# Optimization experiments

Hardware: AMD Instinct MI355X
Metric: run time of the kernel (lower is better)

## Reference

```python
import jax, jax.numpy as jnp
import numpy as np

V = 100000   # num_vertices
E = 3200000  # directed edges (symmetric: both directions of E//2 undirected edges)
B = 8        # batch of meshes
C = 3        # xyz vertex features


def setup_inputs() -> dict:
    key = jax.random.key(0)
    k1, k2, k3, k4 = jax.random.split(key, 4)
    src = jax.random.randint(k1, (E // 2,), 0, V, dtype=jnp.int32)
    dst = jax.random.randint(k2, (E // 2,), 0, V, dtype=jnp.int32)
    edge_index = jnp.stack([jnp.concatenate([src, dst]),
                            jnp.concatenate([dst, src])])  # (2, E)
    features = jax.random.normal(k3, (B, V, C), dtype=jnp.float32)
    target_features = jax.random.normal(k4, (B, V, C), dtype=jnp.float32)
    return {"features": features, "target_features": target_features,
            "edge_index": edge_index}


def _sym_laplacian(edge_index, num_nodes, dtype):
    """get_laplacian(..., normalization='sym'): L = I - D^{-1/2} A D^{-1/2}.
    Returns (lap_row, lap_col, lap_weight) as edge list with self-loops appended."""
    row, col = edge_index
    ones = jnp.ones(row.shape, dtype)
    deg = jax.ops.segment_sum(ones, row, num_segments=num_nodes)
    deg_inv_sqrt = jnp.where(deg > 0, deg, 1.0) ** -0.5
    deg_inv_sqrt = jnp.where(deg > 0, deg_inv_sqrt, 0.0)
    ew = -deg_inv_sqrt[row] * deg_inv_sqrt[col]
    loop = jnp.arange(num_nodes, dtype=row.dtype)
    lap_row = jnp.concatenate([row, loop])
    lap_col = jnp.concatenate([col, loop])
    lap_w = jnp.concatenate([ew, jnp.ones((num_nodes,), dtype)])
    return lap_row, lap_col, lap_w


def _apply_laplacian(x, lap_row, lap_col, lap_w, num_nodes):
    # x: (B, V, C) -> gather on source vertex, scale, scatter_add on target vertex
    xt = jnp.swapaxes(x, 0, 1)                       # (V, B, C)
    msg = xt[lap_row] * lap_w[:, None, None]          # (E+V, B, C)
    out = jax.ops.segment_sum(msg, lap_col, num_segments=num_nodes)  # (V, B, C)
    return jnp.swapaxes(out, 0, 1)                    # (B, V, C)


def reference(features, target_features, edge_index):
    lap_row, lap_col, lap_w = _sym_laplacian(edge_index, V, features.dtype)
    lap_x = _apply_laplacian(features, lap_row, lap_col, lap_w, V)
    lap_y = _apply_laplacian(target_features, lap_row, lap_col, lap_w, V)
    # per-batch mse averaged over batch == global mean since shapes are uniform
    return jnp.mean((lap_x - lap_y) ** 2)
```

## Files before the change

kernel.cpp:

```cpp
#include <hip/hip_runtime.h>

#define C_CONST 3
#define B_CONST 8
#define BC 24
#define NCH 3
#define VP 196
#define NP 512
#define CAP 6784
#define K1_T 1024
#define K1_EPT 16
#define K1_EPB (K1_T * K1_EPT)
#define GT 576
#define KREG 12

typedef float floatx2 __attribute__((ext_vector_type(2)));

__global__ __launch_bounds__(1024) void bucket_kernel(
    const int* __restrict__ row, const int* __restrict__ col, int E,
    int* __restrict__ pcount, unsigned int* __restrict__ bucket)
{
    __shared__ unsigned int sl[K1_EPB];
    __shared__ int hist[NP];
    __shared__ int offs[NP];
    __shared__ int gbase[NP];
    __shared__ int scanbuf[NP];
    int tid = threadIdx.x;
    for (int i = tid; i < NP; i += K1_T) hist[i] = 0;
    __syncthreads();

    int e0 = blockIdx.x * K1_EPB + tid * K1_EPT;
    unsigned int pk[K1_EPT];
    int pe[K1_EPT];
    int rk[K1_EPT];
    if (e0 + K1_EPT <= E) {
        int rs[K1_EPT], cs[K1_EPT];
#pragma unroll
        for (int q = 0; q < K1_EPT / 4; q++) {
            int4 rv = *(const int4*)(row + e0 + q * 4);
            int4 cv = *(const int4*)(col + e0 + q * 4);
            rs[q*4+0] = rv.x; rs[q*4+1] = rv.y; rs[q*4+2] = rv.z; rs[q*4+3] = rv.w;
            cs[q*4+0] = cv.x; cs[q*4+1] = cv.y; cs[q*4+2] = cv.z; cs[q*4+3] = cv.w;
        }
#pragma unroll
        for (int i = 0; i < K1_EPT; i++) {
            int c = cs[i];
            int p = c / VP;
            pe[i] = p;
            pk[i] = (unsigned int)rs[i] | ((unsigned int)(c - p * VP) << 17);
        }
    } else {
#pragma unroll
        for (int i = 0; i < K1_EPT; i++) {
            int e = e0 + i;
            if (e < E) {
                int c = col[e];
                int p = c / VP;
                pe[i] = p;
                pk[i] = (unsigned int)row[e] | ((unsigned int)(c - p * VP) << 17);
            } else { pe[i] = -1; pk[i] = 0; }
        }
    }
#pragma unroll
    for (int i = 0; i < K1_EPT; i++)
        rk[i] = (pe[i] >= 0) ? atomicAdd(&hist[pe[i]], 1) : 0;
    __syncthreads();

    if (tid < NP) scanbuf[tid] = hist[tid];
    __syncthreads();
    for (int off = 1; off < NP; off <<= 1) {
        int t2 = (tid < NP && tid >= off) ? scanbuf[tid - off] : 0;
        __syncthreads();
        if (tid < NP) scanbuf[tid] += t2;
        __syncthreads();
    }
    if (tid < NP) {
        offs[tid] = scanbuf[tid] - hist[tid];
        gbase[tid] = (hist[tid] > 0) ? atomicAdd(&pcount[tid], hist[tid]) : 0;
    }
    __syncthreads();

#pragma unroll
    for (int i = 0; i < K1_EPT; i++)
        if (pe[i] >= 0) sl[offs[pe[i]] + rk[i]] = pk[i];
    __syncthreads();

    int wid = tid >> 6;
    int lane = tid & 63;
    for (int pp = wid * (NP / 16); pp < (wid + 1) * (NP / 16); pp++) {
        int cnt = hist[pp];
        int lo = offs[pp];
        int gb = gbase[pp];
        unsigned int* dst = bucket + (size_t)pp * CAP;
        for (int i = lane; i < cnt; i += 64) {
            int pos = gb + i;
            if (pos < CAP) dst[pos] = sl[lo + i];
        }
    }
}

#define PREP_T 1024
__global__ __launch_bounds__(1024) void prep_kernel(
    const int* __restrict__ pcount, const unsigned int* __restrict__ bucket,
    const float* __restrict__ x, const float* __restrict__ y, int V,
    unsigned char* __restrict__ wh)
{
    __shared__ int cnt[VP];
    __shared__ float ssc[VP];
    __shared__ unsigned char tile[VP * BC];
    int p = blockIdx.x;
    int tid = threadIdx.x;
    for (int i = tid; i < VP; i += PREP_T) cnt[i] = 0;
    __syncthreads();
    int n = pcount[p]; if (n > CAP) n = CAP;
    const unsigned int* bp = bucket + (size_t)p * CAP;
    for (int i = tid; i < n; i += PREP_T) atomicAdd(&cnt[bp[i] >> 17], 1);
    __syncthreads();
    int vb = p * VP;
    int nv = V - vb; if (nv > VP) nv = VP; if (nv < 0) nv = 0;
    for (int i = tid; i < nv; i += PREP_T) {
        int dg = cnt[i];
        ssc[i] = (dg > 0) ? rsqrtf((float)dg) : 1.0f;
    }
    __syncthreads();

    int ns = nv * C_CONST;
    int ns4 = ns >> 2;
    for (int idx = tid; idx < B_CONST * ns4; idx += PREP_T) {
        int b = idx / ns4;
        int q = idx - b * ns4;
        size_t off = ((size_t)b * V + vb) * C_CONST + (size_t)q * 4;
        float4 xv = *(const float4*)(x + off);
        float4 yv = *(const float4*)(y + off);
        float vals[4] = {xv.x - yv.x, xv.y - yv.y, xv.z - yv.z, xv.w - yv.w};
        int f0 = q * 4;
#pragma unroll
        for (int j = 0; j < 4; j++) {
            int f = f0 + j;
            int vl = f / C_CONST;
            int c = f - vl * C_CONST;
            float w = ssc[vl] * vals[j];
            int packed = __builtin_amdgcn_cvt_pk_fp8_f32(w, w, 0, false);
            tile[vl * BC + b * C_CONST + c] = (unsigned char)(packed & 0xFF);
        }
    }
    __syncthreads();

    int nbytes = nv * BC;
    uint4* dst = (uint4*)(wh + (size_t)vb * BC);
    const uint4* srcT = (const uint4*)tile;
    for (int i = tid; i < (nbytes >> 4); i += PREP_T) dst[i] = srcT[i];
}

__global__ __launch_bounds__(GT) void gather_loss_kernel(
    const int* __restrict__ pcount, const unsigned int* __restrict__ bucket,
    const uint2* __restrict__ whp, int V, float inv_n, float* __restrict__ out)
{
    __shared__ unsigned int sorted[CAP];
    __shared__ int rowptr[VP + 1];
    __shared__ int cur[VP];
    __shared__ int scanbuf[256];
    __shared__ float ls[16];
    int p = blockIdx.x;
    int tid = threadIdx.x;
    int n = pcount[p]; if (n > CAP) n = CAP;
    const unsigned int* bp = bucket + (size_t)p * CAP;

    unsigned int ent[KREG];
#pragma unroll
    for (int k = 0; k < KREG; k++) {
        int i = tid + k * GT;
        ent[k] = (i < n) ? bp[i] : 0xFFFFFFFFu;
    }

    for (int i = tid; i < VP; i += GT) cur[i] = 0;
    __syncthreads();
#pragma unroll
    for (int k = 0; k < KREG; k++)
        if (ent[k] != 0xFFFFFFFFu) atomicAdd(&cur[ent[k] >> 17], 1);
    __syncthreads();

    if (tid < 256) scanbuf[tid] = (tid < VP) ? cur[tid] : 0;
    __syncthreads();
    for (int off = 1; off < 256; off <<= 1) {
        int t2 = (tid < 256 && tid >= off) ? scanbuf[tid - off] : 0;
        __syncthreads();
        if (tid < 256) scanbuf[tid] += t2;
        __syncthreads();
    }
    if (tid == 0) rowptr[0] = 0;
    if (tid < VP) rowptr[tid + 1] = scanbuf[tid];
    for (int i = tid; i < VP; i += GT) cur[i] = 0;
    __syncthreads();

#pragma unroll
    for (int k = 0; k < KREG; k++) {
        unsigned int e = ent[k];
        if (e != 0xFFFFFFFFu) {
            int cl = e >> 17;
            int slot = rowptr[cl] + atomicAdd(&cur[cl], 1);
            sorted[slot] = e & 0x1FFFFu;
        }
    }
    __syncthreads();

    float s = 0.0f;
    for (int item = tid; item < VP * NCH; item += GT) {
        int cl = item / NCH;
        int j = item - cl * NCH;
        int v = p * VP + cl;
        if (v < V) {
            int q0 = rowptr[cl], q1 = rowptr[cl + 1];
            int dg = q1 - q0;
            float a0=0.f,a1=0.f,a2=0.f,a3=0.f,a4=0.f,a5=0.f,a6=0.f,a7=0.f;
            for (int q = q0; q < q1; q++) {
                int r = (int)sorted[q];
                uint2 u = whp[r * NCH + j];
                floatx2 f0 = __builtin_amdgcn_cvt_pk_f32_fp8((int)u.x, false);
                floatx2 f1 = __builtin_amdgcn_cvt_pk_f32_fp8((int)u.x, true);
                floatx2 f2 = __builtin_amdgcn_cvt_pk_f32_fp8((int)u.y, false);
                floatx2 f3 = __builtin_amdgcn_cvt_pk_f32_fp8((int)u.y, true);
                a0 += f0.x; a1 += f0.y; a2 += f1.x; a3 += f1.y;
                a4 += f2.x; a5 += f2.y; a6 += f3.x; a7 += f3.y;
            }
            float dvv = (dg > 0) ? rsqrtf((float)dg) : 0.0f;
            float di  = (dg > 0) ? sqrtf((float)dg)  : 1.0f;
            uint2 su = whp[v * NCH + j];
            floatx2 s0 = __builtin_amdgcn_cvt_pk_f32_fp8((int)su.x, false);
            floatx2 s1 = __builtin_amdgcn_cvt_pk_f32_fp8((int)su.x, true);
            floatx2 s2 = __builtin_amdgcn_cvt_pk_f32_fp8((int)su.y, false);
            floatx2 s3 = __builtin_amdgcn_cvt_pk_f32_fp8((int)su.y, true);
            float r0 = s0.x * di - dvv * a0;
            float r1 = s0.y * di - dvv * a1;
            float r2 = s1.x * di - dvv * a2;
            float r3 = s1.y * di - dvv * a3;
            float r4 = s2.x * di - dvv * a4;
            float r5 = s2.y * di - dvv * a5;
            float r6 = s3.x * di - dvv * a6;
            float r7 = s3.y * di - dvv * a7;
            s += r0*r0 + r1*r1 + r2*r2 + r3*r3 + r4*r4 + r5*r5 + r6*r6 + r7*r7;
        }
    }

    for (int off = 32; off > 0; off >>= 1) s += __shfl_down(s, off, 64);
    int lane = tid & 63;
    int wid  = tid >> 6;
    if (lane == 0) ls[wid] = s;
    __syncthreads();
    if (tid == 0) {
        float tot = 0.0f;
        for (int i = 0; i < (GT >> 6); i++) tot += ls[i];
        atomicAdd(out, tot * inv_n);
    }
}

extern "C" void kernel_launch(void* const* d_in, const int* in_sizes, int n_in,
                              void* d_out, int out_size, void* d_ws, size_t ws_size,
                              hipStream_t stream) {
    const float* x = (const float*)d_in[0];
    const float* y = (const float*)d_in[1];
    const int*  ei = (const int*)d_in[2];

    const int E = in_sizes[2] / 2;
    const int V = in_sizes[0] / (B_CONST * C_CONST);
    const int* row = ei;
    const int* col = ei + E;

    char* ws = (char*)d_ws;
    size_t off = 0;
    unsigned int* bucket = (unsigned int*)(ws + off); off += (size_t)NP * CAP * 4;
    unsigned char* wh = (unsigned char*)(ws + off);   off += (size_t)NP * VP * BC;
    int*   pcount = (int*)(ws + off);    off += (size_t)NP * 4;
    float* outf = (float*)d_out;

    hipMemsetAsync(pcount, 0, (size_t)NP * sizeof(int), stream);
    hipMemsetAsync(d_out, 0, sizeof(float), stream);

    bucket_kernel<<<(E + K1_EPB - 1) / K1_EPB, K1_T, 0, stream>>>(row, col, E, pcount, bucket);
    prep_kernel<<<NP, PREP_T, 0, stream>>>(pcount, bucket, x, y, V, wh);
    gather_loss_kernel<<<NP, GT, 0, stream>>>(pcount, bucket, (const uint2*)wh, V,
                                              1.0f / (float)(V * BC), outf);
}
```

Measured before the change: 142.3 us.

## Fuse bucket, prep and gather-loss stages into one cooperative kernel with grid syncs

Replaces the three separate kernel launches with a single cooperative kernel of 256 blocks of 1024 threads. The stages are separated by grid-wide syncs, and each block handles two vertex partitions in the prep and gather stages. The goal is to remove launch gaps and inter-kernel drain. In exchange it adds grid barrier cost, lowers the block count, and loses the coalesced int4 edge loads in the bucketing stage.

After: 217.1 us. 1.53x slower.

```diff
diff --git a/kernel.cpp b/kernel.cpp
--- a/kernel.cpp
+++ b/kernel.cpp
@@ -1,255 +1,248 @@
 #include <hip/hip_runtime.h>
+#include <hip/hip_cooperative_groups.h>
+
+namespace cg = cooperative_groups;
 
 #define C_CONST 3
 #define B_CONST 8
 #define BC 24
 #define NCH 3
 #define VP 196
+#define VP2 392
 #define NP 512
 #define CAP 6784
-#define K1_T 1024
-#define K1_EPT 16
-#define K1_EPB (K1_T * K1_EPT)
-#define GT 576
-#define KREG 12
+#define GRID 256
+#define TPB 1024
+#define EPB 12500
+#define EPT 13
+#define KREG 14
+
+#define SMEM_BYTES 59536
 
 typedef float floatx2 __attribute__((ext_vector_type(2)));
 
-__global__ __launch_bounds__(1024) void bucket_kernel(
+__global__ __launch_bounds__(TPB) void fused_kernel(
     const int* __restrict__ row, const int* __restrict__ col, int E,
-    int* __restrict__ pcount, unsigned int* __restrict__ bucket)
+    int* __restrict__ pcount, unsigned int* __restrict__ bucket,
+    const float* __restrict__ x, const float* __restrict__ y, int V,
+    unsigned char* __restrict__ wh, float* __restrict__ out, float inv_n)
 {
-    __shared__ unsigned int sl[K1_EPB];
-    __shared__ int hist[NP];
-    __shared__ int offs[NP];
-    __shared__ int gbase[NP];
-    __shared__ int scanbuf[NP];
-    int tid = threadIdx.x;
-    for (int i = tid; i < NP; i += K1_T) hist[i] = 0;
-    __syncthreads();
-
-    int e0 = blockIdx.x * K1_EPB + tid * K1_EPT;
-    unsigned int pk[K1_EPT];
-    int pe[K1_EPT];
-    int rk[K1_EPT];
-    if (e0 + K1_EPT <= E) {
-        int rs[K1_EPT], cs[K1_EPT];
-#pragma unroll
-        for (int q = 0; q < K1_EPT / 4; q++) {
-            int4 rv = *(const int4*)(row + e0 + q * 4);
-            int4 cv = *(const int4*)(col + e0 + q * 4);
-            rs[q*4+0] = rv.x; rs[q*4+1] = rv.y; rs[q*4+2] = rv.z; rs[q*4+3] = rv.w;
-            cs[q*4+0] = cv.x; cs[q*4+1] = cv.y; cs[q*4+2] = cv.z; cs[q*4+3] = cv.w;
-        }
-#pragma unroll
-        for (int i = 0; i < K1_EPT; i++) {
-            int c = cs[i];
-            int p = c / VP;
-            pe[i] = p;
-            pk[i] = (unsigned int)rs[i] | ((unsigned int)(c - p * VP) << 17);
-        }
-    } else {
-#pragma unroll
-        for (int i = 0; i < K1_EPT; i++) {
-            int e = e0 + i;
-            if (e < E) {
+    __shared__ __align__(16) unsigned char smem[SMEM_BYTES];
+    cg::grid_group gg = cg::this_grid();
+    const int tid = threadIdx.x;
+    const int b = blockIdx.x;
+
+    {
+        unsigned int* sl = (unsigned int*)smem;
+        int* hist  = (int*)(smem + 50000);
+        int* offs  = (int*)(smem + 52048);
+        int* gbase = (int*)(smem + 54096);
+        int* scan  = (int*)(smem + 56144);
+        for (int i = tid; i < NP; i += TPB) hist[i] = 0;
+        __syncthreads();
+
+        const int ebase = b * EPB;
+        unsigned int pk[EPT]; int pe[EPT]; int rk[EPT];
+#pragma unroll
+        for (int k = 0; k < EPT; k++) {
+            int idx = tid + k * TPB;
+            int e = ebase + idx;
+            if (idx < EPB && e < E) {
                 int c = col[e];
                 int p = c / VP;
-                pe[i] = p;
-                pk[i] = (unsigned int)row[e] | ((unsigned int)(c - p * VP) << 17);
-            } else { pe[i] = -1; pk[i] = 0; }
+                pe[k] = p;
+                pk[k] = (unsigned int)row[e] | ((unsigned int)(c - p * VP) << 17);
+            } else { pe[k] = -1; pk[k] = 0; }
+        }
+#pragma unroll
+        for (int k = 0; k < EPT; k++)
+            rk[k] = (pe[k] >= 0) ? atomicAdd(&hist[pe[k]], 1) : 0;
+        __syncthreads();
+
+        if (tid < NP) scan[tid] = hist[tid];
+        __syncthreads();
+        for (int off = 1; off < NP; off <<= 1) {
+            int t2 = (tid < NP && tid >= off) ? scan[tid - off] : 0;
+            __syncthreads();
+            if (tid < NP) scan[tid] += t2;
+            __syncthreads();
+        }
+        if (tid < NP) {
+            offs[tid] = scan[tid] - hist[tid];
+            gbase[tid] = (hist[tid] > 0) ? atomicAdd(&pcount[tid], hist[tid]) : 0;
+        }
+        __syncthreads();
+#pragma unroll
+        for (int k = 0; k < EPT; k++)
+            if (pe[k] >= 0) sl[offs[pe[k]] + rk[k]] = pk[k];
+        __syncthreads();
+
+        int wid = tid >> 6, lane = tid & 63;
+        for (int pp = wid * (NP / 16); pp < (wid + 1) * (NP / 16); pp++) {
+            int cnt = hist[pp], lo = offs[pp], gb = gbase[pp];
+            unsigned int* dst = bucket + (size_t)pp * CAP;
+            for (int i = lane; i < cnt; i += 64) {
+                int pos = gb + i;
+                if (pos < CAP) dst[pos] = sl[lo + i];
+            }
         }
     }
-#pragma unroll
-    for (int i = 0; i < K1_EPT; i++)
-        rk[i] = (pe[i] >= 0) ? atomicAdd(&hist[pe[i]], 1) : 0;
-    __syncthreads();
-
-    if (tid < NP) scanbuf[tid] = hist[tid];
-    __syncthreads();
-    for (int off = 1; off < NP; off <<= 1) {
-        int t2 = (tid < NP && tid >= off) ? scanbuf[tid - off] : 0;
-        __syncthreads();
-        if (tid < NP) scanbuf[tid] += t2;
-        __syncthreads();
+
+    gg.sync();
+
+    const int p0 = b, p1 = b + GRID;
+    const int vb0 = p0 * VP, vb1 = p1 * VP;
+    int nv0 = V - vb0; nv0 = nv0 < 0 ? 0 : (nv0 > VP ? VP : nv0);
+    int nv1 = V - vb1; nv1 = nv1 < 0 ? 0 : (nv1 > VP ? VP : nv1);
+    int n0 = pcount[p0]; n0 = n0 > CAP ? CAP : n0;
+    int n1 = pcount[p1]; n1 = n1 > CAP ? CAP : n1;
+    const unsigned int* bp0 = bucket + (size_t)p0 * CAP;
+    const unsigned int* bp1 = bucket + (size_t)p1 * CAP;
+    {
+        int* cnt = (int*)smem;
+        float* ssc = (float*)(smem + 1568);
+        unsigned char* tile = smem + 3136;
+        for (int i = tid; i < VP2; i += TPB) cnt[i] = 0;
+        __syncthreads();
+        for (int i = tid; i < n0; i += TPB) atomicAdd(&cnt[bp0[i] >> 17], 1);
+        for (int i = tid; i < n1; i += TPB) atomicAdd(&cnt[VP + (bp1[i] >> 17)], 1);
+        __syncthreads();
+        for (int i = tid; i < VP2; i += TPB) {
+            int dg = cnt[i];
+            ssc[i] = (dg > 0) ? rsqrtf((float)dg) : 1.0f;
+        }
+        __syncthreads();
+#pragma unroll
+        for (int h = 0; h < 2; h++) {
+            int vb = h ? vb1 : vb0;
+            int nv = h ? nv1 : nv0;
+            int ns4 = (nv * C_CONST) >> 2;
+            for (int idx = tid; idx < B_CONST * ns4; idx += TPB) {
+                int b8 = idx / ns4;
+                int q = idx - b8 * ns4;
+                size_t off = ((size_t)b8 * V + vb) * C_CONST + (size_t)q * 4;
+                float4 xv = *(const float4*)(x + off);
+                float4 yv = *(const float4*)(y + off);
+                float vals[4] = {xv.x - yv.x, xv.y - yv.y, xv.z - yv.z, xv.w - yv.w};
+                int f0 = q * 4;
+#pragma unroll
+                for (int j = 0; j < 4; j++) {
+                    int f = f0 + j;
+                    int vl = f / C_CONST;
+                    int c = f - vl * C_CONST;
+                    float w = ssc[h * VP + vl] * vals[j];
+                    int packed = __builtin_amdgcn_cvt_pk_fp8_f32(w, w, 0, false);
+                    tile[(h * VP + vl) * BC + b8 * C_CONST + c] = (unsigned char)(packed & 0xFF);
+                }
+            }
+        }
+        __syncthreads();
+#pragma unroll
+        for (int h = 0; h < 2; h++) {
+            int vb = h ? vb1 : vb0;
+            int nv = h ? nv1 : nv0;
+            int nbytes = nv * BC;
+            uint4* dst = (uint4*)(wh + (size_t)vb * BC);
+            const uint4* srcT = (const uint4*)(tile + h * VP * BC);
+            for (int i = tid; i < (nbytes >> 4); i += TPB) dst[i] = srcT[i];
+        }
     }
-    if (tid < NP) {
-        offs[tid] = scanbuf[tid] - hist[tid];
-        gbase[tid] = (hist[tid] > 0) ? atomicAdd(&pcount[tid], hist[tid]) : 0;
-    }
-    __syncthreads();
-
-#pragma unroll
-    for (int i = 0; i < K1_EPT; i++)
-        if (pe[i] >= 0) sl[offs[pe[i]] + rk[i]] = pk[i];
-    __syncthreads();
-
-    int wid = tid >> 6;
-    int lane = tid & 63;
-    for (int pp = wid * (NP / 16); pp < (wid + 1) * (NP / 16); pp++) {
-        int cnt = hist[pp];
-        int lo = offs[pp];
-        int gb = gbase[pp];
-        unsigned int* dst = bucket + (size_t)pp * CAP;
-        for (int i = lane; i < cnt; i += 64) {
-            int pos = gb + i;
-            if (pos < CAP) dst[pos] = sl[lo + i];
-        }
-    }
-}
-
-#define PREP_T 1024
-__global__ __launch_bounds__(1024) void prep_kernel(
-    const int* __restrict__ pcount, const unsigned int* __restrict__ bucket,
-    const float* __restrict__ x, const float* __restrict__ y, int V,
-    unsigned char* __restrict__ wh)
-{
-    __shared__ int cnt[VP];
-    __shared__ float ssc[VP];
-    __shared__ unsigned char tile[VP * BC];
-    int p = blockIdx.x;
-    int tid = threadIdx.x;
-    for (int i = tid; i < VP; i += PREP_T) cnt[i] = 0;
-    __syncthreads();
-    int n = pcount[p]; if (n > CAP) n = CAP;
-    const unsigned int* bp = bucket + (size_t)p * CAP;
-    for (int i = tid; i < n; i += PREP_T) atomicAdd(&cnt[bp[i] >> 17], 1);
-    __syncthreads();
-    int vb = p * VP;
-    int nv = V - vb; if (nv > VP) nv = VP; if (nv < 0) nv = 0;
-    for (int i = tid; i < nv; i += PREP_T) {
-        int dg = cnt[i];
-        ssc[i] = (dg > 0) ? rsqrtf((float)dg) : 1.0f;
-    }
-    __syncthreads();
-
-    int ns = nv * C_CONST;
-    int ns4 = ns >> 2;
-    for (int idx = tid; idx < B_CONST * ns4; idx += PREP_T) {
-        int b = idx / ns4;
-        int q = idx - b * ns4;
-        size_t off = ((size_t)b * V + vb) * C_CONST + (size_t)q * 4;
-        float4 xv = *(const float4*)(x + off);
-        float4 yv = *(const float4*)(y + off);
-        float vals[4] = {xv.x - yv.x, xv.y - yv.y, xv.z - yv.z, xv.w - yv.w};
-        int f0 = q * 4;
-#pragma unroll
-        for (int j = 0; j < 4; j++) {
-            int f = f0 + j;
-            int vl = f / C_CONST;
-            int c = f - vl * C_CONST;
-            float w = ssc[vl] * vals[j];
-            int packed = __builtin_amdgcn_cvt_pk_fp8_f32(w, w, 0, false);
-            tile[vl * BC + b * C_CONST + c] = (unsigned char)(packed & 0xFF);
-        }
-    }
-    __syncthreads();
-
-    int nbytes = nv * BC;
-    uint4* dst = (uint4*)(wh + (size_t)vb * BC);
-    const uint4* srcT = (const uint4*)tile;
-    for (int i = tid; i < (nbytes >> 4); i += PREP_T) dst[i] = srcT[i];
-}
-
-__global__ __launch_bounds__(GT) void gather_loss_kernel(
-    const int* __restrict__ pcount, const unsigned int* __restrict__ bucket,
-    const uint2* __restrict__ whp, int V, float inv_n, float* __restrict__ out)
-{
-    __shared__ unsigned int sorted[CAP];
-    __shared__ int rowptr[VP + 1];
-    __shared__ int cur[VP];
-    __shared__ int scanbuf[256];
-    __shared__ float ls[16];
-    int p = blockIdx.x;
-    int tid = threadIdx.x;
-    int n = pcount[p]; if (n > CAP) n = CAP;
-    const unsigned int* bp = bucket + (size_t)p * CAP;
-
-    unsigned int ent[KREG];
-#pragma unroll
-    for (int k = 0; k < KREG; k++) {
-        int i = tid + k * GT;
-        ent[k] = (i < n) ? bp[i] : 0xFFFFFFFFu;
-    }
-
-    for (int i = tid; i < VP; i += GT) cur[i] = 0;
-    __syncthreads();
-#pragma unroll
-    for (int k = 0; k < KREG; k++)
-        if (ent[k] != 0xFFFFFFFFu) atomicAdd(&cur[ent[k] >> 17], 1);
-    __syncthreads();
-
-    if (tid < 256) scanbuf[tid] = (tid < VP) ? cur[tid] : 0;
-    __syncthreads();
-    for (int off = 1; off < 256; off <<= 1) {
-        int t2 = (tid < 256 && tid >= off) ? scanbuf[tid - off] : 0;
-        __syncthreads();
-        if (tid < 256) scanbuf[tid] += t2;
-        __syncthreads();
-    }
-    if (tid == 0) rowptr[0] = 0;
-    if (tid < VP) rowptr[tid + 1] = scanbuf[tid];
-    for (int i = tid; i < VP; i += GT) cur[i] = 0;
-    __syncthreads();
-
-#pragma unroll
-    for (int k = 0; k < KREG; k++) {
-        unsigned int e = ent[k];
-        if (e != 0xFFFFFFFFu) {
-            int cl = e >> 17;
-            int slot = rowptr[cl] + atomicAdd(&cur[cl], 1);
-            sorted[slot] = e & 0x1FFFFu;
-        }
-    }
-    __syncthreads();
-
-    float s = 0.0f;
-    for (int item = tid; item < VP * NCH; item += GT) {
-        int cl = item / NCH;
-        int j = item - cl * NCH;
-        int v = p * VP + cl;
-        if (v < V) {
-            int q0 = rowptr[cl], q1 = rowptr[cl + 1];
-            int dg = q1 - q0;
-            float a0=0.f,a1=0.f,a2=0.f,a3=0.f,a4=0.f,a5=0.f,a6=0.f,a7=0.f;
-            for (int q = q0; q < q1; q++) {
-                int r = (int)sorted[q];
-                uint2 u = whp[r * NCH + j];
-                floatx2 f0 = __builtin_amdgcn_cvt_pk_f32_fp8((int)u.x, false);
-                floatx2 f1 = __builtin_amdgcn_cvt_pk_f32_fp8((int)u.x, true);
-                floatx2 f2 = __builtin_amdgcn_cvt_pk_f32_fp8((int)u.y, false);
-                floatx2 f3 = __builtin_amdgcn_cvt_pk_f32_fp8((int)u.y, true);
-                a0 += f0.x; a1 += f0.y; a2 += f1.x; a3 += f1.y;
-                a4 += f2.x; a5 += f2.y; a6 += f3.x; a7 += f3.y;
-            }
-            float dvv = (dg > 0) ? rsqrtf((float)dg) : 0.0f;
-            float di  = (dg > 0) ? sqrtf((float)dg)  : 1.0f;
-            uint2 su = whp[v * NCH + j];
-            floatx2 s0 = __builtin_amdgcn_cvt_pk_f32_fp8((int)su.x, false);
-            floatx2 s1 = __builtin_amdgcn_cvt_pk_f32_fp8((int)su.x, true);
-            floatx2 s2 = __builtin_amdgcn_cvt_pk_f32_fp8((int)su.y, false);
-            floatx2 s3 = __builtin_amdgcn_cvt_pk_f32_fp8((int)su.y, true);
-            float r0 = s0.x * di - dvv * a0;
-            float r1 = s0.y * di - dvv * a1;
-            float r2 = s1.x * di - dvv * a2;
-            float r3 = s1.y * di - dvv * a3;
-            float r4 = s2.x * di - dvv * a4;
-            float r5 = s2.y * di - dvv * a5;
-            float r6 = s3.x * di - dvv * a6;
-            float r7 = s3.y * di - dvv * a7;
-            s += r0*r0 + r1*r1 + r2*r2 + r3*r3 + r4*r4 + r5*r5 + r6*r6 + r7*r7;
-        }
-    }
-
-    for (int off = 32; off > 0; off >>= 1) s += __shfl_down(s, off, 64);
-    int lane = tid & 63;
-    int wid  = tid >> 6;
-    if (lane == 0) ls[wid] = s;
-    __syncthreads();
-    if (tid == 0) {
-        float tot = 0.0f;
-        for (int i = 0; i < (GT >> 6); i++) tot += ls[i];
-        atomicAdd(out, tot * inv_n);
+
+    gg.sync();
+
+    {
+        unsigned int* sorted = (unsigned int*)smem;
+        int* rowptr = (int*)(smem + 54272);
+        int* cur    = (int*)(smem + 55844);
+        int* scan   = (int*)(smem + 57412);
+        float* ls   = (float*)(smem + 59460);
+        const int n = n0 + n1;
+
+        unsigned int ent[KREG];
+#pragma unroll
+        for (int k = 0; k < KREG; k++) {
+            int i = tid + k * TPB;
+            unsigned int e = 0xFFFFFFFFu;
+            if (i < n0) e = bp0[i];
+            else if (i < n) e = bp1[i - n0] + ((unsigned int)VP << 17);
+            ent[k] = e;
+        }
+        for (int i = tid; i < VP2; i += TPB) cur[i] = 0;
+        __syncthreads();
+#pragma unroll
+        for (int k = 0; k < KREG; k++)
+            if (ent[k] != 0xFFFFFFFFu) atomicAdd(&cur[ent[k] >> 17], 1);
+        __syncthreads();
+        if (tid < NP) scan[tid] = (tid < VP2) ? cur[tid] : 0;
+        __syncthreads();
+        for (int off = 1; off < NP; off <<= 1) {
+            int t2 = (tid < NP && tid >= off) ? scan[tid - off] : 0;
+            __syncthreads();
+            if (tid < NP) scan[tid] += t2;
+            __syncthreads();
+        }
+        if (tid == 0) rowptr[0] = 0;
+        if (tid < VP2) rowptr[tid + 1] = scan[tid];
+        for (int i = tid; i < VP2; i += TPB) cur[i] = 0;
+        __syncthreads();
+#pragma unroll
+        for (int k = 0; k < KREG; k++) {
+            unsigned int e = ent[k];
+            if (e != 0xFFFFFFFFu) {
+                int cl = e >> 17;
+                int slot = rowptr[cl] + atomicAdd(&cur[cl], 1);
+                sorted[slot] = e & 0x1FFFFu;
+            }
+        }
+        __syncthreads();
+
+        const uint2* whp = (const uint2*)wh;
+        float s = 0.0f;
+        for (int item = tid; item < VP2 * NCH; item += TPB) {
+            int cl = item / NCH;
+            int j = item - cl * NCH;
+            int v = (cl < VP) ? (vb0 + cl) : (vb1 + cl - VP);
+            if (v < V) {
+                int q0 = rowptr[cl], q1 = rowptr[cl + 1];
+                int dg = q1 - q0;
+                float a0=0.f,a1=0.f,a2=0.f,a3=0.f,a4=0.f,a5=0.f,a6=0.f,a7=0.f;
+                for (int q = q0; q < q1; q++) {
+                    int r = (int)sorted[q];
+                    uint2 u = whp[r * NCH + j];
+                    floatx2 f0 = __builtin_amdgcn_cvt_pk_f32_fp8((int)u.x, false);
+                    floatx2 f1 = __builtin_amdgcn_cvt_pk_f32_fp8((int)u.x, true);
+                    floatx2 f2 = __builtin_amdgcn_cvt_pk_f32_fp8((int)u.y, false);
+                    floatx2 f3 = __builtin_amdgcn_cvt_pk_f32_fp8((int)u.y, true);
+                    a0 += f0.x; a1 += f0.y; a2 += f1.x; a3 += f1.y;
+                    a4 += f2.x; a5 += f2.y; a6 += f3.x; a7 += f3.y;
+                }
+                float dvv = (dg > 0) ? rsqrtf((float)dg) : 0.0f;
+                float di  = (dg > 0) ? sqrtf((float)dg)  : 1.0f;
+                uint2 su = whp[v * NCH + j];
+                floatx2 s0 = __builtin_amdgcn_cvt_pk_f32_fp8((int)su.x, false);
+                floatx2 s1 = __builtin_amdgcn_cvt_pk_f32_fp8((int)su.x, true);
+                floatx2 s2 = __builtin_amdgcn_cvt_pk_f32_fp8((int)su.y, false);
+                floatx2 s3 = __builtin_amdgcn_cvt_pk_f32_fp8((int)su.y, true);
+                float r0 = s0.x * di - dvv * a0;
+                float r1 = s0.y * di - dvv * a1;
+                float r2 = s1.x * di - dvv * a2;
+                float r3 = s1.y * di - dvv * a3;
+                float r4 = s2.x * di - dvv * a4;
+                float r5 = s2.y * di - dvv * a5;
+                float r6 = s3.x * di - dvv * a6;
+                float r7 = s3.y * di - dvv * a7;
+                s += r0*r0 + r1*r1 + r2*r2 + r3*r3 + r4*r4 + r5*r5 + r6*r6 + r7*r7;
+            }
+        }
+        for (int off = 32; off > 0; off >>= 1) s += __shfl_down(s, off, 64);
+        int lane = tid & 63, wid = tid >> 6;
+        if (lane == 0) ls[wid] = s;
+        __syncthreads();
+        if (tid == 0) {
+            float tot = 0.0f;
+            for (int i = 0; i < TPB / 64; i++) tot += ls[i];
+            atomicAdd(out, tot * inv_n);
+        }
     }
 }
 
@@ -269,14 +262,15 @@
     size_t off = 0;
     unsigned int* bucket = (unsigned int*)(ws + off); off += (size_t)NP * CAP * 4;
     unsigned char* wh = (unsigned char*)(ws + off);   off += (size_t)NP * VP * BC;
-    int*   pcount = (int*)(ws + off);    off += (size_t)NP * 4;
+    int* pcount = (int*)(ws + off);                   off += (size_t)NP * 4;
     float* outf = (float*)d_out;
 
     hipMemsetAsync(pcount, 0, (size_t)NP * sizeof(int), stream);
     hipMemsetAsync(d_out, 0, sizeof(float), stream);
 
-    bucket_kernel<<<(E + K1_EPB - 1) / K1_EPB, K1_T, 0, stream>>>(row, col, E, pcount, bucket);
-    prep_kernel<<<NP, PREP_T, 0, stream>>>(pcount, bucket, x, y, V, wh);
-    gather_loss_kernel<<<NP, GT, 0, stream>>>(pcount, bucket, (const uint2*)wh, V,
-                                              1.0f / (float)(V * BC), outf);
+    int Ei = E, Vi = V;
+    float inv_n = 1.0f / (float)(V * BC);
+    void* args[] = {(void*)&row, (void*)&col, (void*)&Ei, (void*)&pcount, (void*)&bucket,
+                    (void*)&x, (void*)&y, (void*)&Vi, (void*)&wh, (void*)&outf, (void*)&inv_n};
+    hipLaunchCooperativeKernel((void*)fused_kernel, dim3(GRID), dim3(TPB), args, 0, stream);
 }
```

## Split per-vertex gather across two lanes and retune bucket/gather block sizes

Applied to the files above, without the earlier changes.

The gather-loss kernel now gives each (vertex, channel) item to two adjacent lanes, which each sum half the neighbour list and combine partial sums with a shuffle. The inner loop is unrolled by two so more loads are in flight, and the block size goes from 576 to 1024 threads with fewer register-held entries per thread. The bucket kernel drops to 512 threads so each thread owns one partition, and it does the histogram atomics inline while packing partition and rank into one word to save registers. The aim is more memory parallelism and less divergence from uneven degrees, at the cost of extra shuffles and half-idle lanes in the final step.

Result: faster. 138.9 us (-2.4%).

```diff
diff --git a/kernel.cpp b/kernel.cpp
--- a/kernel.cpp
+++ b/kernel.cpp
@@ -7,15 +7,15 @@
 #define VP 196
 #define NP 512
 #define CAP 6784
-#define K1_T 1024
+#define K1_T 512
 #define K1_EPT 16
 #define K1_EPB (K1_T * K1_EPT)
-#define GT 576
-#define KREG 12
+#define GT 1024
+#define KREG 7
 
 typedef float floatx2 __attribute__((ext_vector_type(2)));
 
-__global__ __launch_bounds__(1024) void bucket_kernel(
+__global__ __launch_bounds__(K1_T) void bucket_kernel(
     const int* __restrict__ row, const int* __restrict__ col, int E,
     int* __restrict__ pcount, unsigned int* __restrict__ bucket)
 {
@@ -25,28 +25,28 @@
     __shared__ int gbase[NP];
     __shared__ int scanbuf[NP];
     int tid = threadIdx.x;
-    for (int i = tid; i < NP; i += K1_T) hist[i] = 0;
+    hist[tid] = 0;
     __syncthreads();
 
     int e0 = blockIdx.x * K1_EPB + tid * K1_EPT;
     unsigned int pk[K1_EPT];
-    int pe[K1_EPT];
-    int rk[K1_EPT];
+    unsigned int pack[K1_EPT];
     if (e0 + K1_EPT <= E) {
-        int rs[K1_EPT], cs[K1_EPT];
 #pragma unroll
         for (int q = 0; q < K1_EPT / 4; q++) {
             int4 rv = *(const int4*)(row + e0 + q * 4);
             int4 cv = *(const int4*)(col + e0 + q * 4);
-            rs[q*4+0] = rv.x; rs[q*4+1] = rv.y; rs[q*4+2] = rv.z; rs[q*4+3] = rv.w;
-            cs[q*4+0] = cv.x; cs[q*4+1] = cv.y; cs[q*4+2] = cv.z; cs[q*4+3] = cv.w;
-        }
-#pragma unroll
-        for (int i = 0; i < K1_EPT; i++) {
-            int c = cs[i];
-            int p = c / VP;
-            pe[i] = p;
-            pk[i] = (unsigned int)rs[i] | ((unsigned int)(c - p * VP) << 17);
+            int rr[4] = {rv.x, rv.y, rv.z, rv.w};
+            int cc[4] = {cv.x, cv.y, cv.z, cv.w};
+#pragma unroll
+            for (int j = 0; j < 4; j++) {
+                int i = q * 4 + j;
+                int c = cc[j];
+                int p = c / VP;
+                pk[i] = (unsigned int)rr[j] | ((unsigned int)(c - p * VP) << 17);
+                int rk = atomicAdd(&hist[p], 1);
+                pack[i] = (unsigned int)p | ((unsigned int)rk << 9);
+            }
         }
     } else {
 #pragma unroll
@@ -55,41 +55,37 @@
             if (e < E) {
                 int c = col[e];
                 int p = c / VP;
-                pe[i] = p;
                 pk[i] = (unsigned int)row[e] | ((unsigned int)(c - p * VP) << 17);
-            } else { pe[i] = -1; pk[i] = 0; }
-        }
-    }
-#pragma unroll
-    for (int i = 0; i < K1_EPT; i++)
-        rk[i] = (pe[i] >= 0) ? atomicAdd(&hist[pe[i]], 1) : 0;
-    __syncthreads();
-
-    if (tid < NP) scanbuf[tid] = hist[tid];
+                int rk = atomicAdd(&hist[p], 1);
+                pack[i] = (unsigned int)p | ((unsigned int)rk << 9);
+            } else { pk[i] = 0; pack[i] = 0xFFFFFFFFu; }
+        }
+    }
+    __syncthreads();
+
+    scanbuf[tid] = hist[tid];
     __syncthreads();
     for (int off = 1; off < NP; off <<= 1) {
-        int t2 = (tid < NP && tid >= off) ? scanbuf[tid - off] : 0;
+        int t2 = (tid >= off) ? scanbuf[tid - off] : 0;
         __syncthreads();
-        if (tid < NP) scanbuf[tid] += t2;
+        scanbuf[tid] += t2;
         __syncthreads();
     }
-    if (tid < NP) {
-        offs[tid] = scanbuf[tid] - hist[tid];
-        gbase[tid] = (hist[tid] > 0) ? atomicAdd(&pcount[tid], hist[tid]) : 0;
-    }
-    __syncthreads();
-
-#pragma unroll
-    for (int i = 0; i < K1_EPT; i++)
-        if (pe[i] >= 0) sl[offs[pe[i]] + rk[i]] = pk[i];
-    __syncthreads();
-
-    int wid = tid >> 6;
-    int lane = tid & 63;
-    for (int pp = wid * (NP / 16); pp < (wid + 1) * (NP / 16); pp++) {
-        int cnt = hist[pp];
-        int lo = offs[pp];
-        int gb = gbase[pp];
+    offs[tid] = scanbuf[tid] - hist[tid];
+    gbase[tid] = (hist[tid] > 0) ? atomicAdd(&pcount[tid], hist[tid]) : 0;
+    __syncthreads();
+
+#pragma unroll
+    for (int i = 0; i < K1_EPT; i++) {
+        unsigned int pc = pack[i];
+        if (pc != 0xFFFFFFFFu)
+            sl[offs[pc & 511u] + (pc >> 9)] = pk[i];
+    }
+    __syncthreads();
+
+    int wid = tid >> 6, lane = tid & 63;
+    for (int pp = wid * (NP / 8); pp < (wid + 1) * (NP / 8); pp++) {
+        int cnt = hist[pp], lo = offs[pp], gb = gbase[pp];
         unsigned int* dst = bucket + (size_t)pp * CAP;
         for (int i = lane; i < cnt; i += 64) {
             int pos = gb + i;
@@ -99,7 +95,7 @@
 }
 
 #define PREP_T 1024
-__global__ __launch_bounds__(1024) void prep_kernel(
+__global__ __launch_bounds__(PREP_T) void prep_kernel(
     const int* __restrict__ pcount, const unsigned int* __restrict__ bucket,
     const float* __restrict__ x, const float* __restrict__ y, int V,
     unsigned char* __restrict__ wh)
@@ -204,51 +200,79 @@
     __syncthreads();
 
     float s = 0.0f;
-    for (int item = tid; item < VP * NCH; item += GT) {
-        int cl = item / NCH;
-        int j = item - cl * NCH;
+    for (int item = tid; item < VP * NCH * 2; item += GT) {
+        int pi = item >> 1, h = item & 1;
+        int cl = pi / NCH;
+        int j = pi - cl * NCH;
         int v = p * VP + cl;
         if (v < V) {
             int q0 = rowptr[cl], q1 = rowptr[cl + 1];
             int dg = q1 - q0;
+            int qm = q0 + ((dg + 1) >> 1);
+            int qa = h ? qm : q0;
+            int qb = h ? q1 : qm;
             float a0=0.f,a1=0.f,a2=0.f,a3=0.f,a4=0.f,a5=0.f,a6=0.f,a7=0.f;
-            for (int q = q0; q < q1; q++) {
-                int r = (int)sorted[q];
-                uint2 u = whp[r * NCH + j];
-                floatx2 f0 = __builtin_amdgcn_cvt_pk_f32_fp8((int)u.x, false);
-                floatx2 f1 = __builtin_amdgcn_cvt_pk_f32_fp8((int)u.x, true);
-                floatx2 f2 = __builtin_amdgcn_cvt_pk_f32_fp8((int)u.y, false);
-                floatx2 f3 = __builtin_amdgcn_cvt_pk_f32_fp8((int)u.y, true);
+            int q = qa;
+            for (; q + 2 <= qb; q += 2) {
+                int r0 = (int)sorted[q];
+                int r1 = (int)sorted[q + 1];
+                uint2 u0 = whp[r0 * NCH + j];
+                uint2 u1 = whp[r1 * NCH + j];
+                floatx2 f0 = __builtin_amdgcn_cvt_pk_f32_fp8((int)u0.x, false);
+                floatx2 f1 = __builtin_amdgcn_cvt_pk_f32_fp8((int)u0.x, true);
+                floatx2 f2 = __builtin_amdgcn_cvt_pk_f32_fp8((int)u0.y, false);
+                floatx2 f3 = __builtin_amdgcn_cvt_pk_f32_fp8((int)u0.y, true);
+                a0 += f0.x; a1 += f0.y; a2 += f1.x; a3 += f1.y;
+                a4 += f2.x; a5 += f2.y; a6 += f3.x; a7 += f3.y;
+                floatx2 g0 = __builtin_amdgcn_cvt_pk_f32_fp8((int)u1.x, false);
+                floatx2 g1 = __builtin_amdgcn_cvt_pk_f32_fp8((int)u1.x, true);
+                floatx2 g2 = __builtin_amdgcn_cvt_pk_f32_fp8((int)u1.y, false);
+                floatx2 g3 = __builtin_amdgcn_cvt_pk_f32_fp8((int)u1.y, true);
+                a0 += g0.x; a1 += g0.y; a2 += g1.x; a3 += g1.y;
+                a4 += g2.x; a5 += g2.y; a6 += g3.x; a7 += g3.y;
+            }
+            if (q < qb) {
+                int r0 = (int)sorted[q];
+                uint2 u0 = whp[r0 * NCH + j];
+                floatx2 f0 = __builtin_amdgcn_cvt_pk_f32_fp8((int)u0.x, false);
+                floatx2 f1 = __builtin_amdgcn_cvt_pk_f32_fp8((int)u0.x, true);
+                floatx2 f2 = __builtin_amdgcn_cvt_pk_f32_fp8((int)u0.y, false);
+                floatx2 f3 = __builtin_amdgcn_cvt_pk_f32_fp8((int)u0.y, true);
                 a0 += f0.x; a1 += f0.y; a2 += f1.x; a3 += f1.y;
                 a4 += f2.x; a5 += f2.y; a6 += f3.x; a7 += f3.y;
             }
-            float dvv = (dg > 0) ? rsqrtf((float)dg) : 0.0f;
-            float di  = (dg > 0) ? sqrtf((float)dg)  : 1.0f;
-            uint2 su = whp[v * NCH + j];
-            floatx2 s0 = __builtin_amdgcn_cvt_pk_f32_fp8((int)su.x, false);
-            floatx2 s1 = __builtin_amdgcn_cvt_pk_f32_fp8((int)su.x, true);
-            floatx2 s2 = __builtin_amdgcn_cvt_pk_f32_fp8((int)su.y, false);
-            floatx2 s3 = __builtin_amdgcn_cvt_pk_f32_fp8((int)su.y, true);
-            float r0 = s0.x * di - dvv * a0;
-            float r1 = s0.y * di - dvv * a1;
-            float r2 = s1.x * di - dvv * a2;
-            float r3 = s1.y * di - dvv * a3;
-            float r4 = s2.x * di - dvv * a4;
-            float r5 = s2.y * di - dvv * a5;
-            float r6 = s3.x * di - dvv * a6;
-            float r7 = s3.y * di - dvv * a7;
-            s += r0*r0 + r1*r1 + r2*r2 + r3*r3 + r4*r4 + r5*r5 + r6*r6 + r7*r7;
+            a0 += __shfl_xor(a0, 1, 64); a1 += __shfl_xor(a1, 1, 64);
+            a2 += __shfl_xor(a2, 1, 64); a3 += __shfl_xor(a3, 1, 64);
+            a4 += __shfl_xor(a4, 1, 64); a5 += __shfl_xor(a5, 1, 64);
+            a6 += __shfl_xor(a6, 1, 64); a7 += __shfl_xor(a7, 1, 64);
+            if (h == 0) {
+                float dvv = (dg > 0) ? rsqrtf((float)dg) : 0.0f;
+                float di  = (dg > 0) ? sqrtf((float)dg)  : 1.0f;
+                uint2 su = whp[v * NCH + j];
+                floatx2 s0 = __builtin_amdgcn_cvt_pk_f32_fp8((int)su.x, false);
+                floatx2 s1 = __builtin_amdgcn_cvt_pk_f32_fp8((int)su.x, true);
+                floatx2 s2 = __builtin_amdgcn_cvt_pk_f32_fp8((int)su.y, false);
+                floatx2 s3 = __builtin_amdgcn_cvt_pk_f32_fp8((int)su.y, true);
+                float r0 = s0.x * di - dvv * a0;
+                float r1 = s0.y * di - dvv * a1;
+                float r2 = s1.x * di - dvv * a2;
+                float r3 = s1.y * di - dvv * a3;
+                float r4 = s2.x * di - dvv * a4;
+                float r5 = s2.y * di - dvv * a5;
+                float r6 = s3.x * di - dvv * a6;
+                float r7 = s3.y * di - dvv * a7;
+                s += r0*r0 + r1*r1 + r2*r2 + r3*r3 + r4*r4 + r5*r5 + r6*r6 + r7*r7;
+            }
         }
     }
 
     for (int off = 32; off > 0; off >>= 1) s += __shfl_down(s, off, 64);
-    int lane = tid & 63;
-    int wid  = tid >> 6;
+    int lane = tid & 63, wid = tid >> 6;
     if (lane == 0) ls[wid] = s;
     __syncthreads();
     if (tid == 0) {
         float tot = 0.0f;
-        for (int i = 0; i < (GT >> 6); i++) tot += ls[i];
+        for (int i = 0; i < GT / 64; i++) tot += ls[i];
         atomicAdd(out, tot * inv_n);
     }
 }
@@ -269,7 +293,7 @@
     size_t off = 0;
     unsigned int* bucket = (unsigned int*)(ws + off); off += (size_t)NP * CAP * 4;
     unsigned char* wh = (unsigned char*)(ws + off);   off += (size_t)NP * VP * BC;
-    int*   pcount = (int*)(ws + off);    off += (size_t)NP * 4;
+    int* pcount = (int*)(ws + off);                   off += (size_t)NP * 4;
     float* outf = (float*)d_out;
 
     hipMemsetAsync(pcount, 0, (size_t)NP * sizeof(int), stream);
```
